# Optimization experiments

Hardware: AMD Instinct MI355X
Metric: run time of the kernel (lower is better)

The kernel has to match this reference:

```python
import jax, jax.numpy as jnp
import numpy as np

B, K, C = 8192, 64, 8  # batch, feature dim, number of private-attribute classes


def setup_inputs() -> dict:
    key = jax.random.key(0)
    k1, k2, k3 = jax.random.split(key, 3)
    mu = jax.random.normal(k1, (B, K), dtype=jnp.float32)
    private_attribute = jax.random.randint(k2, (B,), 0, C)
    A = jax.random.normal(k3, (K, K), dtype=jnp.float32) * 0.05
    cov = A @ A.T + jnp.eye(K, dtype=jnp.float32)  # SPD prior covariance
    return {"mu": mu, "private_attribute": private_attribute, "cov": cov}


def _kldiv(mu1, S1, mu2, S2, k):
    # KL( N(mu1,S1) || N(mu2,S2) )
    d = mu2 - mu1
    tr = jnp.trace(jnp.linalg.solve(S2, S1))       # tr(inv(S2) S1)
    quad = d @ jnp.linalg.solve(S2, d)             # d^T inv(S2) d
    ld2 = jnp.linalg.slogdet(S2)[1]
    ld1 = jnp.linalg.slogdet(S1)[1]
    return 0.5 * (tr + quad - k + ld2 - ld1)


def reference(mu, private_attribute, cov):
    Bn, k = mu.shape
    labels = private_attribute
    ones = jnp.ones((Bn,), mu.dtype)
    counts = jax.ops.segment_sum(ones, labels, num_segments=C)                # [C]
    safe = jnp.maximum(counts, 1.0)
    mu_F = jax.ops.segment_sum(mu, labels, num_segments=C) / safe[:, None]    # [C,k] group means
    mu_total = jnp.mean(mu, axis=0)                                           # [k]
    dt = mu - mu_total
    Sigma_total = cov + dt.T @ dt / Bn                                        # [k,k]
    dc = mu - mu_F[labels]                                                    # [B,k]
    outer = jnp.einsum('bi,bj->bij', dc, dc)                                  # [B,k,k]
    Sigma_F = cov + jax.ops.segment_sum(outer, labels, num_segments=C) / safe[:, None, None]  # [C,k,k]
    kl = jax.vmap(lambda m, S: _kldiv(m, S, mu_total, Sigma_total, k))(mu_F, Sigma_F)  # [C]
    # The original loops `for i in range(len(keys)-1)` over dict keys ordered by
    # first occurrence in the batch, i.e. it SKIPS the class whose first sample
    # appears latest. Reproduce that exactly.
    pos = jnp.arange(Bn)
    first_pos = jnp.min(
        jnp.where(labels[:, None] == jnp.arange(C)[None, :], pos[:, None], Bn), axis=0
    )                                                                          # [C]
    present = first_pos < Bn
    last_key = jnp.argmax(jnp.where(present, first_pos, -1))
    w = jnp.where(present & (jnp.arange(C) != last_key), counts, 0.0)          # count_Fs weights
    result = jnp.sum(kl * w * Bn) / (Bn ** 2)
    return result
```

## Files before the change

kernel.cpp:

```cpp
#include <hip/hip_runtime.h>

#define CC 8
#define KK 64
#define BB 8192
#define NCHUNK 16
#define NGBLK (NCHUNK * CC)
#define ROWS_PER_CHUNK (BB / NCHUNK)

#define OFF_G     0
#define OFF_GSUM  262144
#define OFF_GCNT  264192
#define OFF_CNTR  264224
#define OFF_FLG   264228
#define OFF_GFST  264232
#define OFF_INV   264264
#define OFF_LD2   297032
#define OFF_TERMS 297040

#define SM_BUFA  0
#define SM_SPART 4160
#define SM_PANEL 8320
#define SM_LB    8832
#define SM_LDI   12992
#define SM_MB    13056
#define SM_INTS  13120
#define SMEM_BACK 13128

__device__ __forceinline__ double readlane_f64(double v, int lane) {
  union { double d; int i[2]; } u, r;
  u.d = v;
  r.i[0] = __builtin_amdgcn_readlane(u.i[0], lane);
  r.i[1] = __builtin_amdgcn_readlane(u.i[1], lane);
  return r.d;
}

__global__ __launch_bounds__(256) void k_front(const float* __restrict__ mu,
                                               const int* __restrict__ labels, char* ws) {
  __shared__ double smem[2176];
  int blk = blockIdx.x;
  int chunk = blk >> 3, c = blk & 7;
  int tid = threadIdx.x;
  int lane = tid & 63, w = tid >> 6;
  int tx = tid & 15, ty = tid >> 4;
  float* rows = (float*)smem;
  int* labs = (int*)(smem + 2048);
  float* ssum = (float*)(smem + 2080);
  int* scnt = (int*)(smem + 2112);
  int* sfst = (int*)(smem + 2114);
  double* G = (double*)(ws + OFF_G);
  float* gsum = (float*)(ws + OFF_GSUM);
  int* gcount = (int*)(ws + OFF_GCNT);
  int* gfirst = (int*)(ws + OFF_GFST);

  double acc[4][4] = {{0.0}};
  float rsum = 0.f;
  int cnt = 0, first = BB;
  int base = chunk * ROWS_PER_CHUNK;
  const float4* mu4 = (const float4*)mu + (size_t)base * (KK / 4);
  if (tid < KK) ssum[tid] = 0.f;

  float4 pf[4];
  int plab = 0;
#pragma unroll
  for (int i = 0; i < 4; ++i) pf[i] = mu4[tid + i * 256];
  if (tid < 64) plab = labels[base + tid];

#pragma unroll 1
  for (int g = 0; g < ROWS_PER_CHUNK / 64; ++g) {
    __syncthreads();
    float4* rows4 = (float4*)rows;
#pragma unroll
    for (int i = 0; i < 4; ++i) rows4[tid + i * 256] = pf[i];
    if (tid < 64) labs[tid] = plab;
    __syncthreads();
    if (g + 1 < ROWS_PER_CHUNK / 64) {
#pragma unroll
      for (int i = 0; i < 4; ++i) pf[i] = mu4[(g + 1) * 1024 + tid + i * 256];
      if (tid < 64) plab = labels[base + (g + 1) * 64 + tid];
    }
#pragma unroll 4
    for (int r = 0; r < 16; ++r) {
      int rr = w * 16 + r;
      if (labs[rr] == c) rsum += rows[rr * KK + lane];
    }
    if (lane < 16 && labs[w * 16 + lane] == c) {
      cnt++;
      first = min(first, base + g * 64 + w * 16 + lane);
    }
    unsigned long long m = __ballot(labs[lane] == c);
    while (m) {
      int r = __builtin_ctzll(m);
      m &= m - 1;
      const float4* rw4 = (const float4*)(rows + r * KK);
      float4 a4 = rw4[ty], b4 = rw4[tx];
      const float* ai = (const float*)&a4;
      const float* bj = (const float*)&b4;
#pragma unroll
      for (int a = 0; a < 4; ++a)
#pragma unroll
        for (int b = 0; b < 4; ++b) acc[a][b] += (double)ai[a] * (double)bj[b];
    }
  }
  double* Gc = G + (size_t)c * KK * KK;
#pragma unroll
  for (int a = 0; a < 4; ++a)
#pragma unroll
    for (int b = 0; b < 4; ++b)
      atomicAdd(&Gc[(ty * 4 + a) * KK + tx * 4 + b], acc[a][b]);
  atomicAdd(&ssum[lane], rsum);
#pragma unroll
  for (int off = 32; off; off >>= 1) {
    cnt += __shfl_down(cnt, off);
    first = min(first, __shfl_down(first, off));
  }
  if (lane == 0) { scnt[w] = cnt; sfst[w] = first; }
  __syncthreads();
  if (tid < KK) {
    float v = ssum[tid];
    if (v != 0.f) atomicAdd(&gsum[c * KK + tid], v);
  }
  if (tid == 0) {
    int ct = scnt[0] + scnt[1] + scnt[2] + scnt[3];
    if (ct) {
      atomicAdd(&gcount[c], ct);
      atomicMin(&gfirst[c], min(min(sfst[0], sfst[1]), min(sfst[2], sfst[3])));
    }
  }
}

__device__ __noinline__ double chol64(double* smem, bool isS2) {
  int tid = threadIdx.x;
  int t = tid & 63, w = tid >> 6;
  double (*A)[KK + 1] = (double (*)[KK + 1])(smem + SM_BUFA);
  double (*Lb)[KK + 1] = (double (*)[KK + 1])(smem + SM_LB);
  double* Ldi = smem + SM_LDI;
  double ldacc = 0.0;
  int bound = t | 7;
#pragma unroll 1
  for (int p = 0; p < 8; ++p) {
    const int P0 = p * 8;
    double cc_[8];
#pragma unroll
    for (int m = 0; m < 8; ++m) cc_[m] = A[t][P0 + m];
    double uu[8];
    double pd = 1.0;
#pragma unroll
    for (int m = 0; m < 8; ++m) {
      double akk = readlane_f64(cc_[m], P0 + m);
      pd *= akk;
      double inv;
      asm("v_rcp_f64 %0, %1" : "=v"(inv) : "v"(akk));
      inv = inv * fma(-akk, inv, 2.0);
      uu[m] = cc_[m] * inv;
      if (isS2 && w == 0) {
        double rsv = sqrt(akk) * inv;
        Lb[t][P0 + m] = cc_[m] * rsv;
        if (t == 0) Ldi[P0 + m] = rsv;
      }
#pragma unroll
      for (int mm = m + 1; mm < 8; ++mm)
        cc_[mm] -= uu[m] * readlane_f64(cc_[m], P0 + mm);
    }
    ldacc += log(pd);
#pragma unroll 1
    for (int jb = p + 1 + w; jb < 8; jb += 4) {
      int j = jb * 8;
      if (j <= bound) {
        double aj[8];
#pragma unroll
        for (int q = 0; q < 8; ++q) aj[q] = A[t][j + q];
#pragma unroll
        for (int m = 0; m < 8; ++m) {
          double u = uu[m];
#pragma unroll
          for (int q = 0; q < 8; ++q)
            aj[q] -= u * readlane_f64(cc_[m], j + q);
        }
#pragma unroll
        for (int q = 0; q < 8; ++q) A[t][j + q] = aj[q];
      }
    }
    __syncthreads();
  }
  return ldacc;
}

__global__ __launch_bounds__(256) void k_back(const float* __restrict__ cov,
                                              float* out, char* ws) {
  __shared__ double smem[SMEM_BACK];
  int blk = blockIdx.x;
  int tid = threadIdx.x;
  int t = tid & 63, w = tid >> 6;
  double* G = (double*)(ws + OFF_G);
  float* gsum = (float*)(ws + OFF_GSUM);
  int* gcount = (int*)(ws + OFF_GCNT);
  int* gfirst = (int*)(ws + OFF_GFST);
  double* invS2 = (double*)(ws + OFF_INV);
  double* ld2g = (double*)(ws + OFF_LD2);
  double* terms = (double*)(ws + OFF_TERMS);
  int* cntr = (int*)(ws + OFF_CNTR);
  int* flg = (int*)(ws + OFF_FLG);
  double* mb = smem + SM_MB;
  int* cnt8s = (int*)(smem + SM_INTS);
  int* fst8s = cnt8s + 8;

  if (blk < CC) {
    int c = blk;
    if (tid < 64) {
      double st = 0.0;
#pragma unroll
      for (int cc2 = 0; cc2 < CC; ++cc2) st += (double)gsum[cc2 * KK + t];
      smem[SM_LDI + t] = st * (1.0 / (double)BB);
      smem[SM_MB + t] = (double)gsum[c * KK + t];
    } else if (tid < 80) {
      int j = tid - 64;
      if (j < 8) cnt8s[j] = gcount[j];
      else fst8s[j - 8] = gfirst[j - 8];
    }
    __syncthreads();
    int nc = cnt8s[c];
    double ncd = (double)nc;
    double safe = nc > 0 ? ncd : 1.0;
    double inv_safe = 1.0 / safe;
    if (tid < 64) {
      double m = smem[SM_MB + t] * inv_safe;
      smem[SM_MB + t] = m;
      smem[SM_LDI + t] -= m;
    }
    __syncthreads();

    double* stash = smem + SM_LB;
    const double* Gc = G + (size_t)c * KK * KK;
#pragma unroll
    for (int q = 0; q < 16; ++q) {
      int e = tid + q * 256;
      int r = e >> 6, c0 = e & 63;
      double v = (double)cov[e] + (Gc[e] - ncd * mb[r] * mb[c0]) * inv_safe;
      smem[SM_BUFA + r * (KK + 1) + c0] = v;
      stash[r * (KK + 1) + c0] = v;
    }
    __syncthreads();

    double ld1 = chol64(smem, false);

    if (tid == 0) {
      int it = 0;
      while (__hip_atomic_load(flg, __ATOMIC_ACQUIRE, __HIP_MEMORY_SCOPE_AGENT) == 0 &&
             ++it < (1 << 20))
        __builtin_amdgcn_s_sleep(8);
    }
    __syncthreads();
    double ld2 = __hip_atomic_load(ld2g, __ATOMIC_RELAXED, __HIP_MEMORY_SCOPE_AGENT);
    double* dvv = smem + SM_LDI;
    double trp = 0.0, qp = 0.0;
#pragma unroll 4
    for (int rr = 0; rr < 16; ++rr) {
      int r = w * 16 + rr;
      double iv = __hip_atomic_load(&invS2[r * KK + t], __ATOMIC_RELAXED,
                                    __HIP_MEMORY_SCOPE_AGENT);
      trp += iv * stash[r * (KK + 1) + t];
      qp += iv * dvv[r];
    }
    qp *= dvv[t];
#pragma unroll
    for (int m = 32; m; m >>= 1) {
      trp += __shfl_down(trp, m);
      qp += __shfl_down(qp, m);
    }
    double* wred = smem + SM_PANEL;
    if (t == 0) { wred[w * 2] = trp; wred[w * 2 + 1] = qp; }
    __syncthreads();
    if (tid == 0) {
      double tr = wred[0] + wred[2] + wred[4] + wred[6];
      double quad = wred[1] + wred[3] + wred[5] + wred[7];
      int best = 0;
      long long bv = -2;
      for (int j = 0; j < CC; ++j) {
        long long v = cnt8s[j] > 0 ? (long long)fst8s[j] : -1;
        if (v > bv) { bv = v; best = j; }
      }
      double kl = 0.5 * (tr + quad - (double)KK + ld2 - ld1);
      double wgt = (nc > 0 && c != best) ? ncd : 0.0;
      double term = kl * wgt / (double)BB;
      atomicExch((unsigned long long*)&terms[c],
                 (unsigned long long)__double_as_longlong(term));
      __threadfence();
      int old = atomicAdd(cntr, 1);
      if (old == CC - 1) {
        double s = 0.0;
        for (int j = 0; j < CC; ++j) s += atomicAdd(&terms[j], 0.0);
        out[0] = (float)s;
      }
    }
  } else {
    if (tid < 64) {
      double st = 0.0;
#pragma unroll
      for (int cc2 = 0; cc2 < CC; ++cc2) st += (double)gsum[cc2 * KK + t];
      mb[t] = st * (1.0 / (double)BB);
    }
    __syncthreads();
    const double invB = 1.0 / (double)BB;
#pragma unroll 1
    for (int q = 0; q < 16; ++q) {
      int e = tid + q * 256;
      double g = 0.0;
#pragma unroll
      for (int c2 = 0; c2 < CC; ++c2) g += G[(size_t)c2 * KK * KK + e];
      int r = e >> 6, c0 = e & 63;
      smem[SM_BUFA + r * (KK + 1) + c0] = (double)cov[e] + g * invB - mb[r] * mb[c0];
    }
    __syncthreads();
    double ld2 = chol64(smem, true);
    double (*Xs)[KK] = (double (*)[KK])(smem + SM_BUFA);
    double (*Lb)[KK + 1] = (double (*)[KK + 1])(smem + SM_LB);
    double* Ldi = smem + SM_LDI;
    double* spart = smem + SM_SPART;
#pragma unroll 1
    for (int g = 0; g < 8; ++g) {
      int I0 = g * 8;
      double sv[8];
#pragma unroll
      for (int m = 0; m < 8; ++m) sv[m] = 0.0;
#pragma unroll 1
      for (int j = w; j < I0; j += 4) {
        double xj = Xs[j][t];
#pragma unroll
        for (int m = 0; m < 8; ++m) sv[m] += Lb[I0 + m][j] * xj;
      }
#pragma unroll
      for (int m = 0; m < 8; ++m) spart[(w * 8 + m) * 64 + t] = sv[m];
      __syncthreads();
      if (w == 0) {
        double sv2[8];
#pragma unroll
        for (int m = 0; m < 8; ++m)
          sv2[m] = spart[m * 64 + t] + spart[(8 + m) * 64 + t] +
                   spart[(16 + m) * 64 + t] + spart[(24 + m) * 64 + t];
#pragma unroll
        for (int m = 0; m < 8; ++m) {
          int i = I0 + m;
          double x = (((i == t) ? 1.0 : 0.0) - sv2[m]) * Ldi[i];
#pragma unroll
          for (int mm = m + 1; mm < 8; ++mm) sv2[mm] += Lb[I0 + mm][i] * x;
          Xs[i][t] = x;
        }
      }
      __syncthreads();
    }
    {
      double s[16];
#pragma unroll
      for (int rr = 0; rr < 16; ++rr) s[rr] = 0.0;
#pragma unroll 1
      for (int half = 0; half < 2; ++half) {
        double xt[32];
        int kb = half * 32;
#pragma unroll
        for (int kk = 0; kk < 32; ++kk) xt[kk] = Xs[kb + kk][t];
#pragma unroll 1
        for (int rr = 0; rr < 16; ++rr) {
          int r = w + rr * 4;
          double acc2 = 0.0;
#pragma unroll
          for (int kk = 0; kk < 32; ++kk)
            acc2 += readlane_f64(xt[kk], r) * xt[kk];
          s[rr] += acc2;
        }
      }
#pragma unroll 1
      for (int rr = 0; rr < 16; ++rr) {
        int r = w + rr * 4;
        __hip_atomic_store(&invS2[r * KK + t], s[rr], __ATOMIC_RELAXED,
                           __HIP_MEMORY_SCOPE_AGENT);
      }
    }
    __syncthreads();
    if (tid == 0) {
      __hip_atomic_store(ld2g, ld2, __ATOMIC_RELAXED, __HIP_MEMORY_SCOPE_AGENT);
      __threadfence();
      __hip_atomic_store(flg, 1, __ATOMIC_RELEASE, __HIP_MEMORY_SCOPE_AGENT);
    }
  }
}

extern "C" void kernel_launch(void* const* d_in, const int* in_sizes, int n_in,
                              void* d_out, int out_size, void* d_ws, size_t ws_size,
                              hipStream_t stream) {
  (void)in_sizes; (void)n_in; (void)out_size; (void)ws_size;
  const float* mu = (const float*)d_in[0];
  const int* labels = (const int*)d_in[1];
  const float* cov = (const float*)d_in[2];
  float* out = (float*)d_out;
  char* ws = (char*)d_ws;

  hipMemsetAsync(ws, 0, OFF_GFST, stream);
  hipMemsetAsync(ws + OFF_GFST, 0x7f, CC * sizeof(int), stream);

  k_front<<<NGBLK, 256, 0, stream>>>(mu, labels, ws);
  k_back<<<CC + 1, 256, 0, stream>>>(cov, out, ws);
}
```

Before: 111.1 us.

## Fuse front and back kernels into one launch with a completion-counter spin barrier

Merges the accumulation kernel and the Cholesky/KL kernel into a single launch. The back-end blocks spin on a global done counter until all 128 front blocks finish. The S2 block now publishes only the triangular inverse factor X. Each class block forms X^T X itself in parallel, instead of the S2 block computing the full inverse serially. This removes one kernel launch gap and shortens the S2 critical path. In exchange it relies on all blocks being co-resident, which 137 blocks on this GPU should satisfy, and it adds redundant work in each class block.

```diff
diff --git a/kernel.cpp b/kernel.cpp
--- a/kernel.cpp
+++ b/kernel.cpp
@@ -12,10 +12,11 @@
 #define OFF_GCNT  264192
 #define OFF_CNTR  264224
 #define OFF_FLG   264228
-#define OFF_GFST  264232
-#define OFF_INV   264264
-#define OFF_LD2   297032
-#define OFF_TERMS 297040
+#define OFF_DONE  264232
+#define OFF_GFST  264240
+#define OFF_X     264272
+#define OFF_LD2   297040
+#define OFF_TERMS 297048
 
 #define SM_BUFA  0
 #define SM_SPART 4160
@@ -24,7 +25,7 @@
 #define SM_LDI   12992
 #define SM_MB    13056
 #define SM_INTS  13120
-#define SMEM_BACK 13128
+#define SMEM_N   13128
 
 __device__ __forceinline__ double readlane_f64(double v, int lane) {
   union { double d; int i[2]; } u, r;
@@ -33,99 +34,14 @@
   r.i[1] = __builtin_amdgcn_readlane(u.i[1], lane);
   return r.d;
 }
-
-__global__ __launch_bounds__(256) void k_front(const float* __restrict__ mu,
-                                               const int* __restrict__ labels, char* ws) {
-  __shared__ double smem[2176];
-  int blk = blockIdx.x;
-  int chunk = blk >> 3, c = blk & 7;
-  int tid = threadIdx.x;
-  int lane = tid & 63, w = tid >> 6;
-  int tx = tid & 15, ty = tid >> 4;
-  float* rows = (float*)smem;
-  int* labs = (int*)(smem + 2048);
-  float* ssum = (float*)(smem + 2080);
-  int* scnt = (int*)(smem + 2112);
-  int* sfst = (int*)(smem + 2114);
-  double* G = (double*)(ws + OFF_G);
-  float* gsum = (float*)(ws + OFF_GSUM);
-  int* gcount = (int*)(ws + OFF_GCNT);
-  int* gfirst = (int*)(ws + OFF_GFST);
-
-  double acc[4][4] = {{0.0}};
-  float rsum = 0.f;
-  int cnt = 0, first = BB;
-  int base = chunk * ROWS_PER_CHUNK;
-  const float4* mu4 = (const float4*)mu + (size_t)base * (KK / 4);
-  if (tid < KK) ssum[tid] = 0.f;
-
-  float4 pf[4];
-  int plab = 0;
-#pragma unroll
-  for (int i = 0; i < 4; ++i) pf[i] = mu4[tid + i * 256];
-  if (tid < 64) plab = labels[base + tid];
-
-#pragma unroll 1
-  for (int g = 0; g < ROWS_PER_CHUNK / 64; ++g) {
-    __syncthreads();
-    float4* rows4 = (float4*)rows;
-#pragma unroll
-    for (int i = 0; i < 4; ++i) rows4[tid + i * 256] = pf[i];
-    if (tid < 64) labs[tid] = plab;
-    __syncthreads();
-    if (g + 1 < ROWS_PER_CHUNK / 64) {
-#pragma unroll
-      for (int i = 0; i < 4; ++i) pf[i] = mu4[(g + 1) * 1024 + tid + i * 256];
-      if (tid < 64) plab = labels[base + (g + 1) * 64 + tid];
-    }
-#pragma unroll 4
-    for (int r = 0; r < 16; ++r) {
-      int rr = w * 16 + r;
-      if (labs[rr] == c) rsum += rows[rr * KK + lane];
-    }
-    if (lane < 16 && labs[w * 16 + lane] == c) {
-      cnt++;
-      first = min(first, base + g * 64 + w * 16 + lane);
-    }
-    unsigned long long m = __ballot(labs[lane] == c);
-    while (m) {
-      int r = __builtin_ctzll(m);
-      m &= m - 1;
-      const float4* rw4 = (const float4*)(rows + r * KK);
-      float4 a4 = rw4[ty], b4 = rw4[tx];
-      const float* ai = (const float*)&a4;
-      const float* bj = (const float*)&b4;
-#pragma unroll
-      for (int a = 0; a < 4; ++a)
-#pragma unroll
-        for (int b = 0; b < 4; ++b) acc[a][b] += (double)ai[a] * (double)bj[b];
-    }
-  }
-  double* Gc = G + (size_t)c * KK * KK;
-#pragma unroll
-  for (int a = 0; a < 4; ++a)
-#pragma unroll
-    for (int b = 0; b < 4; ++b)
-      atomicAdd(&Gc[(ty * 4 + a) * KK + tx * 4 + b], acc[a][b]);
-  atomicAdd(&ssum[lane], rsum);
-#pragma unroll
-  for (int off = 32; off; off >>= 1) {
-    cnt += __shfl_down(cnt, off);
-    first = min(first, __shfl_down(first, off));
-  }
-  if (lane == 0) { scnt[w] = cnt; sfst[w] = first; }
-  __syncthreads();
-  if (tid < KK) {
-    float v = ssum[tid];
-    if (v != 0.f) atomicAdd(&gsum[c * KK + tid], v);
-  }
-  if (tid == 0) {
-    int ct = scnt[0] + scnt[1] + scnt[2] + scnt[3];
-    if (ct) {
-      atomicAdd(&gcount[c], ct);
-      atomicMin(&gfirst[c], min(min(sfst[0], sfst[1]), min(sfst[2], sfst[3])));
-    }
-  }
+__device__ __forceinline__ double aload_f64(const double* p) {
+  return __hip_atomic_load(p, __ATOMIC_RELAXED, __HIP_MEMORY_SCOPE_AGENT);
+}
+__device__ __forceinline__ float aload_f32(const float* p) {
+  return __hip_atomic_load(p, __ATOMIC_RELAXED, __HIP_MEMORY_SCOPE_AGENT);
+}
+__device__ __forceinline__ int aload_i32(const int* p) {
+  return __hip_atomic_load(p, __ATOMIC_RELAXED, __HIP_MEMORY_SCOPE_AGENT);
 }
 
 __device__ __noinline__ double chol64(double* smem, bool isS2) {
@@ -185,9 +101,11 @@
   return ldacc;
 }
 
-__global__ __launch_bounds__(256) void k_back(const float* __restrict__ cov,
-                                              float* out, char* ws) {
-  __shared__ double smem[SMEM_BACK];
+__global__ __launch_bounds__(256) void k_all(const float* __restrict__ mu,
+                                             const int* __restrict__ labels,
+                                             const float* __restrict__ cov,
+                                             float* out, char* ws) {
+  __shared__ double smem[SMEM_N];
   int blk = blockIdx.x;
   int tid = threadIdx.x;
   int t = tid & 63, w = tid >> 6;
@@ -195,27 +113,129 @@
   float* gsum = (float*)(ws + OFF_GSUM);
   int* gcount = (int*)(ws + OFF_GCNT);
   int* gfirst = (int*)(ws + OFF_GFST);
-  double* invS2 = (double*)(ws + OFF_INV);
+  double* Xg = (double*)(ws + OFF_X);
   double* ld2g = (double*)(ws + OFF_LD2);
   double* terms = (double*)(ws + OFF_TERMS);
   int* cntr = (int*)(ws + OFF_CNTR);
   int* flg = (int*)(ws + OFF_FLG);
+  int* done = (int*)(ws + OFF_DONE);
+
+  if (blk < NGBLK) {
+    int chunk = blk >> 3, c = blk & 7;
+    int lane = tid & 63;
+    int tx = tid & 15, ty = tid >> 4;
+    float* rows = (float*)smem;
+    int* labs = (int*)(smem + 2048);
+    float* ssum = (float*)(smem + 2080);
+    int* scnt = (int*)(smem + 2112);
+    int* sfst = (int*)(smem + 2114);
+
+    double acc[4][4] = {{0.0}};
+    float rsum = 0.f;
+    int cnt = 0, first = BB;
+    int base = chunk * ROWS_PER_CHUNK;
+    const float4* mu4 = (const float4*)mu + (size_t)base * (KK / 4);
+    if (tid < KK) ssum[tid] = 0.f;
+
+    float4 pf[4];
+    int plab = 0;
+#pragma unroll
+    for (int i = 0; i < 4; ++i) pf[i] = mu4[tid + i * 256];
+    if (tid < 64) plab = labels[base + tid];
+
+#pragma unroll 1
+    for (int g = 0; g < ROWS_PER_CHUNK / 64; ++g) {
+      __syncthreads();
+      float4* rows4 = (float4*)rows;
+#pragma unroll
+      for (int i = 0; i < 4; ++i) rows4[tid + i * 256] = pf[i];
+      if (tid < 64) labs[tid] = plab;
+      __syncthreads();
+      if (g + 1 < ROWS_PER_CHUNK / 64) {
+#pragma unroll
+        for (int i = 0; i < 4; ++i) pf[i] = mu4[(g + 1) * 1024 + tid + i * 256];
+        if (tid < 64) plab = labels[base + (g + 1) * 64 + tid];
+      }
+#pragma unroll 4
+      for (int r = 0; r < 16; ++r) {
+        int rr = w * 16 + r;
+        if (labs[rr] == c) rsum += rows[rr * KK + lane];
+      }
+      if (lane < 16 && labs[w * 16 + lane] == c) {
+        cnt++;
+        first = min(first, base + g * 64 + w * 16 + lane);
+      }
+      unsigned long long m = __ballot(labs[lane] == c);
+      while (m) {
+        int r = __builtin_ctzll(m);
+        m &= m - 1;
+        const float4* rw4 = (const float4*)(rows + r * KK);
+        float4 a4 = rw4[ty], b4 = rw4[tx];
+        const float* ai = (const float*)&a4;
+        const float* bj = (const float*)&b4;
+#pragma unroll
+        for (int a = 0; a < 4; ++a)
+#pragma unroll
+          for (int b = 0; b < 4; ++b) acc[a][b] += (double)ai[a] * (double)bj[b];
+      }
+    }
+    double* Gc = G + (size_t)c * KK * KK;
+#pragma unroll
+    for (int a = 0; a < 4; ++a)
+#pragma unroll
+      for (int b = 0; b < 4; ++b)
+        atomicAdd(&Gc[(ty * 4 + a) * KK + tx * 4 + b], acc[a][b]);
+    atomicAdd(&ssum[lane], rsum);
+#pragma unroll
+    for (int off = 32; off; off >>= 1) {
+      cnt += __shfl_down(cnt, off);
+      first = min(first, __shfl_down(first, off));
+    }
+    if (lane == 0) { scnt[w] = cnt; sfst[w] = first; }
+    __syncthreads();
+    if (tid < KK) {
+      float v = ssum[tid];
+      if (v != 0.f) atomicAdd(&gsum[c * KK + tid], v);
+    }
+    if (tid == 0) {
+      int ct = scnt[0] + scnt[1] + scnt[2] + scnt[3];
+      if (ct) {
+        atomicAdd(&gcount[c], ct);
+        atomicMin(&gfirst[c], min(min(sfst[0], sfst[1]), min(sfst[2], sfst[3])));
+      }
+    }
+    __syncthreads();
+    if (tid == 0) {
+      __threadfence();
+      atomicAdd(done, 1);
+    }
+    return;
+  }
+
+  if (tid == 0) {
+    int it = 0;
+    while (__hip_atomic_load(done, __ATOMIC_ACQUIRE, __HIP_MEMORY_SCOPE_AGENT) < NGBLK &&
+           ++it < (1 << 22))
+      __builtin_amdgcn_s_sleep(8);
+  }
+  __syncthreads();
+
   double* mb = smem + SM_MB;
   int* cnt8s = (int*)(smem + SM_INTS);
   int* fst8s = cnt8s + 8;
 
-  if (blk < CC) {
-    int c = blk;
+  if (blk < NGBLK + CC) {
+    int c = blk - NGBLK;
     if (tid < 64) {
       double st = 0.0;
 #pragma unroll
-      for (int cc2 = 0; cc2 < CC; ++cc2) st += (double)gsum[cc2 * KK + t];
+      for (int cc2 = 0; cc2 < CC; ++cc2) st += (double)aload_f32(&gsum[cc2 * KK + t]);
       smem[SM_LDI + t] = st * (1.0 / (double)BB);
-      smem[SM_MB + t] = (double)gsum[c * KK + t];
+      smem[SM_MB + t] = (double)aload_f32(&gsum[c * KK + t]);
     } else if (tid < 80) {
       int j = tid - 64;
-      if (j < 8) cnt8s[j] = gcount[j];
-      else fst8s[j - 8] = gfirst[j - 8];
+      if (j < 8) cnt8s[j] = aload_i32(&gcount[j]);
+      else fst8s[j - 8] = aload_i32(&gfirst[j - 8]);
     }
     __syncthreads();
     int nc = cnt8s[c];
@@ -235,7 +255,7 @@
     for (int q = 0; q < 16; ++q) {
       int e = tid + q * 256;
       int r = e >> 6, c0 = e & 63;
-      double v = (double)cov[e] + (Gc[e] - ncd * mb[r] * mb[c0]) * inv_safe;
+      double v = (double)cov[e] + (aload_f64(&Gc[e]) - ncd * mb[r] * mb[c0]) * inv_safe;
       smem[SM_BUFA + r * (KK + 1) + c0] = v;
       stash[r * (KK + 1) + c0] = v;
     }
@@ -246,20 +266,38 @@
     if (tid == 0) {
       int it = 0;
       while (__hip_atomic_load(flg, __ATOMIC_ACQUIRE, __HIP_MEMORY_SCOPE_AGENT) == 0 &&
-             ++it < (1 << 20))
+             ++it < (1 << 22))
         __builtin_amdgcn_s_sleep(8);
     }
     __syncthreads();
-    double ld2 = __hip_atomic_load(ld2g, __ATOMIC_RELAXED, __HIP_MEMORY_SCOPE_AGENT);
+    double ld2 = aload_f64(ld2g);
+
     double* dvv = smem + SM_LDI;
+    double s[16];
+#pragma unroll
+    for (int rr = 0; rr < 16; ++rr) s[rr] = 0.0;
+#pragma unroll 1
+    for (int half = 0; half < 2; ++half) {
+      double xt[32];
+      int kb = half * 32;
+#pragma unroll
+      for (int kk = 0; kk < 32; ++kk) xt[kk] = aload_f64(&Xg[(kb + kk) * KK + t]);
+#pragma unroll 1
+      for (int rr = 0; rr < 16; ++rr) {
+        int r = w + rr * 4;
+        double acc2 = 0.0;
+#pragma unroll
+        for (int kk = 0; kk < 32; ++kk)
+          acc2 += readlane_f64(xt[kk], r) * xt[kk];
+        s[rr] += acc2;
+      }
+    }
     double trp = 0.0, qp = 0.0;
-#pragma unroll 4
+#pragma unroll
     for (int rr = 0; rr < 16; ++rr) {
-      int r = w * 16 + rr;
-      double iv = __hip_atomic_load(&invS2[r * KK + t], __ATOMIC_RELAXED,
-                                    __HIP_MEMORY_SCOPE_AGENT);
-      trp += iv * stash[r * (KK + 1) + t];
-      qp += iv * dvv[r];
+      int r = w + rr * 4;
+      trp += s[rr] * stash[r * (KK + 1) + t];
+      qp += s[rr] * dvv[r];
     }
     qp *= dvv[t];
 #pragma unroll
@@ -287,16 +325,16 @@
       __threadfence();
       int old = atomicAdd(cntr, 1);
       if (old == CC - 1) {
-        double s = 0.0;
-        for (int j = 0; j < CC; ++j) s += atomicAdd(&terms[j], 0.0);
-        out[0] = (float)s;
+        double sres = 0.0;
+        for (int j = 0; j < CC; ++j) sres += atomicAdd(&terms[j], 0.0);
+        out[0] = (float)sres;
       }
     }
   } else {
     if (tid < 64) {
       double st = 0.0;
 #pragma unroll
-      for (int cc2 = 0; cc2 < CC; ++cc2) st += (double)gsum[cc2 * KK + t];
+      for (int cc2 = 0; cc2 < CC; ++cc2) st += (double)aload_f32(&gsum[cc2 * KK + t]);
       mb[t] = st * (1.0 / (double)BB);
     }
     __syncthreads();
@@ -306,12 +344,13 @@
       int e = tid + q * 256;
       double g = 0.0;
 #pragma unroll
-      for (int c2 = 0; c2 < CC; ++c2) g += G[(size_t)c2 * KK * KK + e];
+      for (int c2 = 0; c2 < CC; ++c2) g += aload_f64(&G[(size_t)c2 * KK * KK + e]);
       int r = e >> 6, c0 = e & 63;
       smem[SM_BUFA + r * (KK + 1) + c0] = (double)cov[e] + g * invB - mb[r] * mb[c0];
     }
     __syncthreads();
     double ld2 = chol64(smem, true);
+
     double (*Xs)[KK] = (double (*)[KK])(smem + SM_BUFA);
     double (*Lb)[KK + 1] = (double (*)[KK + 1])(smem + SM_LB);
     double* Ldi = smem + SM_LDI;
@@ -348,32 +387,11 @@
       }
       __syncthreads();
     }
-    {
-      double s[16];
-#pragma unroll
-      for (int rr = 0; rr < 16; ++rr) s[rr] = 0.0;
-#pragma unroll 1
-      for (int half = 0; half < 2; ++half) {
-        double xt[32];
-        int kb = half * 32;
-#pragma unroll
-        for (int kk = 0; kk < 32; ++kk) xt[kk] = Xs[kb + kk][t];
-#pragma unroll 1
-        for (int rr = 0; rr < 16; ++rr) {
-          int r = w + rr * 4;
-          double acc2 = 0.0;
-#pragma unroll
-          for (int kk = 0; kk < 32; ++kk)
-            acc2 += readlane_f64(xt[kk], r) * xt[kk];
-          s[rr] += acc2;
-        }
-      }
-#pragma unroll 1
-      for (int rr = 0; rr < 16; ++rr) {
-        int r = w + rr * 4;
-        __hip_atomic_store(&invS2[r * KK + t], s[rr], __ATOMIC_RELAXED,
-                           __HIP_MEMORY_SCOPE_AGENT);
-      }
+#pragma unroll 1
+    for (int ii = 0; ii < 16; ++ii) {
+      int i = w * 16 + ii;
+      __hip_atomic_store(&Xg[i * KK + t], Xs[i][t], __ATOMIC_RELAXED,
+                         __HIP_MEMORY_SCOPE_AGENT);
     }
     __syncthreads();
     if (tid == 0) {
@@ -397,6 +415,5 @@
   hipMemsetAsync(ws, 0, OFF_GFST, stream);
   hipMemsetAsync(ws + OFF_GFST, 0x7f, CC * sizeof(int), stream);
 
-  k_front<<<NGBLK, 256, 0, stream>>>(mu, labels, ws);
-  k_back<<<CC + 1, 256, 0, stream>>>(cov, out, ws);
-}
+  k_all<<<NGBLK + CC + 1, 256, 0, stream>>>(mu, labels, cov, out, ws);
+}
```

Result: slower. 116.1 us (+4.5%).
